# Kernel optimization log

Measured on AMD Instinct MI355X. Metric: run time of the kernel, lower is better.

The kernel has to match this reference:

```python
import jax, jax.numpy as jnp
import numpy as np

B, T, F, H = 2048, 50, 256, 256
PREVIOUS_VISIT = 50  # number of recurrence steps


def setup_inputs() -> dict:
    key = jax.random.key(0)
    k1, k2, k3, k4 = jax.random.split(key, 4)
    scale = 0.05  # keep gates in a sane range
    return {
        "input_context": jax.random.normal(k1, (B, T, F), dtype=jnp.float32),
        "W": jax.random.normal(k2, (F, 4 * H), dtype=jnp.float32) * scale,
        "U": jax.random.normal(k3, (H, 4 * H), dtype=jnp.float32) * scale,
        "b": jax.random.normal(k4, (4 * H,), dtype=jnp.float32) * scale,
    }


def reference(input_context, W, U, b):
    # Keras LSTMCell math, gate order i, f, g(cell candidate), o.
    batch = input_context.shape[0]
    hidden = U.shape[0]
    h0 = jnp.zeros((batch, hidden), dtype=input_context.dtype)
    c0 = jnp.zeros((batch, hidden), dtype=input_context.dtype)

    def step(carry, x_t):
        h, c = carry
        z = x_t @ W + h @ U + b  # [B, 4H]
        i, f, g, o = jnp.split(z, 4, axis=-1)
        i = jax.nn.sigmoid(i)
        f = jax.nn.sigmoid(f)
        g = jnp.tanh(g)
        o = jax.nn.sigmoid(o)
        c_new = f * c + i * g
        h_new = o * jnp.tanh(c_new)
        return (h_new, c_new), None

    # scan over time: [PV, B, F]
    xs = jnp.swapaxes(input_context[:, :PREVIOUS_VISIT, :], 0, 1)
    (h_fin, c_fin), _ = jax.lax.scan(step, (h0, c0), xs)
    # original returns (output_forward, state_forward=[h, c]); h == output
    return h_fin, c_fin
```

## Files before the change

### kernel.cpp

```cpp
#include <hip/hip_runtime.h>


#define B_ 2048
#define T_ 50
#define F_ 256
#define H_ 256
#define NZ 1024

typedef __attribute__((ext_vector_type(8))) short short8;
typedef __attribute__((ext_vector_type(4))) float f32x4;
typedef __attribute__((ext_vector_type(4))) int i32x4;
typedef unsigned short ushort_t;
typedef unsigned int uint_t;

__device__ __forceinline__ ushort_t f2bf(float f) {
    uint_t u = __float_as_uint(f);
    return (ushort_t)((u + 0x7FFFu + ((u >> 16) & 1u)) >> 16);
}
__device__ __forceinline__ uint_t pack2bf(float lo, float hi) {
    return (uint_t)f2bf(lo) | ((uint_t)f2bf(hi) << 16);
}
__device__ __forceinline__ float bf2f(ushort_t u) {
    return __uint_as_float(((uint_t)u) << 16);
}
__device__ __forceinline__ float sigm(float z) {
    return __builtin_amdgcn_rcpf(1.0f + __builtin_amdgcn_exp2f(z * -1.44269504f));
}
__device__ __forceinline__ float tanh_f(float z) {
    return 2.0f * __builtin_amdgcn_rcpf(1.0f + __builtin_amdgcn_exp2f(z * -2.88539008f)) - 1.0f;
}
__device__ __forceinline__ float xz_at(uint2 u, int j) {
    uint_t v = (j < 2) ? u.x : u.y;
    v = (j & 1) ? (v >> 16) : (v & 0xFFFFu);
    return bf2f((ushort_t)v);
}

__global__ void pack_w(const float* __restrict__ Wm, ushort_t* __restrict__ W2) {
    int gid  = blockIdx.x * 256 + threadIdx.x;
    int lane = gid & 63;
    int nf   = (gid >> 6) & 7;
    int w    = (gid >> 9) & 7;
    int kf   = (gid >> 12) & 7;
    int col = (nf >> 1) * 256 + w * 32 + (nf & 1) * 16 + (lane & 15);
    int kb  = kf * 32 + (lane >> 4) * 8;
    short8 v;
#pragma unroll
    for (int e = 0; e < 8; ++e)
        v[e] = (short)f2bf(Wm[(size_t)(kb + e) * NZ + col]);
    *(short8*)(W2 + ((((size_t)kf * 8 + w) * 8 + nf) * 64 + lane) * 8) = v;
}

__global__ void pack_scale(const float* __restrict__ Um,
                           float* __restrict__ scq, float* __restrict__ scd) {
    int j    = (blockIdx.x * 256 + threadIdx.x) >> 6;
    int lane = threadIdx.x & 63;
    float mx = 0.f;
#pragma unroll
    for (int i = 0; i < H_ / 64; ++i)
        mx = fmaxf(mx, fabsf(Um[(size_t)(i * 64 + lane) * NZ + j]));
#pragma unroll
    for (int off = 32; off; off >>= 1)
        mx = fmaxf(mx, __shfl_down(mx, off));
    if (lane == 0) {
        scq[j] = (mx > 0.f) ? (127.0f / mx) : 0.f;
        scd[j] = mx * (1.0f / 16129.0f);
    }
}

__global__ void pack_u8(const float* __restrict__ Um,
                        const float* __restrict__ scq, char* __restrict__ U8) {
    int gid  = blockIdx.x * 256 + threadIdx.x;
    int lane = gid & 63;
    int nf   = (gid >> 6) & 7;
    int w    = (gid >> 9) & 7;
    int kf   = (gid >> 12) & 3;
    int col = (nf >> 1) * 256 + w * 32 + (nf & 1) * 16 + (lane & 15);
    int k0  = kf * 64 + (lane >> 4) * 16;
    float qs = scq[col];
    union { char c[16]; int4 v; } u;
#pragma unroll
    for (int e = 0; e < 16; ++e)
        u.c[e] = (char)__float2int_rn(Um[(size_t)(k0 + e) * NZ + col] * qs);
    *(int4*)(U8 + (((size_t)(kf * 8 + w) * 8 + nf) << 10) + (size_t)lane * 16) = u.v;
}

__global__ __launch_bounds__(512, 2) void xw_gemm(
    const float* __restrict__ x, const float* __restrict__ bias,
    const ushort_t* __restrict__ W2, ushort_t* __restrict__ xz2) {
    __shared__ __align__(16) ushort_t As[64 * 256];

    const int tid = threadIdx.x;
    const int t = blockIdx.x, rb = blockIdx.y, row0 = rb * 64;
    const int w = tid >> 6, lane = tid & 63, r16 = lane & 15, q = lane >> 4;

    {
        int sr = tid >> 4, sc = tid & 15;
#pragma unroll
        for (int rr = 0; rr < 64; rr += 32) {
            const float* xp = x + ((size_t)(row0 + rr + sr) * T_ + t) * F_ + sc * 16;
            float4 f0 = *(const float4*)(xp + 0);
            float4 f1 = *(const float4*)(xp + 4);
            float4 f2 = *(const float4*)(xp + 8);
            float4 f3 = *(const float4*)(xp + 12);
            uint4 u0 = {pack2bf(f0.x, f0.y), pack2bf(f0.z, f0.w),
                        pack2bf(f1.x, f1.y), pack2bf(f1.z, f1.w)};
            uint4 u1 = {pack2bf(f2.x, f2.y), pack2bf(f2.z, f2.w),
                        pack2bf(f3.x, f3.y), pack2bf(f3.z, f3.w)};
            int c0 = (2 * sc) ^ (sr & 7), c1 = (2 * sc + 1) ^ (sr & 7);
            *(uint4*)&As[(rr + sr) * 256 + c0 * 8] = u0;
            *(uint4*)&As[(rr + sr) * 256 + c1 * 8] = u1;
        }
    }
    float bcol[8];
#pragma unroll
    for (int nf = 0; nf < 8; ++nf)
        bcol[nf] = bias[(nf >> 1) * 256 + w * 32 + (nf & 1) * 16 + r16];
    __syncthreads();

    f32x4 acc[4][8];
#pragma unroll
    for (int m = 0; m < 4; ++m)
#pragma unroll
        for (int nf = 0; nf < 8; ++nf) acc[m][nf] = (f32x4){0.f, 0.f, 0.f, 0.f};
    short8 SB0[8], SB1[8];

#define LOADB(BUF, KF_)                                                       \
    _Pragma("unroll") for (int nf = 0; nf < 8; ++nf)                          \
        BUF[nf] = *(const short8*)(W2 +                                       \
            ((((size_t)(KF_) * 8 + w) * 8 + nf) * 64 + lane) * 8);

#define MF1(BUF, KF_)                                                         \
    do {                                                                      \
        _Pragma("unroll") for (int m = 0; m < 4; ++m) {                       \
            short8 a_ = *(const short8*)&As[(m * 16 + r16) * 256              \
                                            + (((KF_)*4 + q) ^ (r16 & 7)) * 8];\
            _Pragma("unroll") for (int nf = 0; nf < 8; ++nf)                  \
                acc[m][nf] = __builtin_amdgcn_mfma_f32_16x16x32_bf16(         \
                    a_, BUF[nf], acc[m][nf], 0, 0, 0);                        \
        }                                                                     \
    } while (0)

    LOADB(SB0, 0); LOADB(SB1, 1);
    MF1(SB0, 0); LOADB(SB0, 2);
    MF1(SB1, 1); LOADB(SB1, 3);
    MF1(SB0, 2); LOADB(SB0, 4);
    MF1(SB1, 3); LOADB(SB1, 5);
    MF1(SB0, 4); LOADB(SB0, 6);
    MF1(SB1, 5); LOADB(SB1, 7);
    MF1(SB0, 6);
    MF1(SB1, 7);

    uint2* outp = (uint2*)xz2;
#pragma unroll
    for (int m = 0; m < 4; ++m) {
        const size_t cb = (((size_t)t * 64 + (size_t)(rb * 2 + (m >> 1))) * 8 + w) * 16
                        + (size_t)(m & 1) * 8;
#pragma unroll
        for (int nf = 0; nf < 8; ++nf) {
            f32x4 a = acc[m][nf];
            float b = bcol[nf];
            uint2 o = {pack2bf(a[0] + b, a[1] + b), pack2bf(a[2] + b, a[3] + b)};
            outp[(cb + nf) * 64 + lane] = o;
        }
    }
#undef LOADB
#undef MF1
}

__global__ __launch_bounds__(512, 1) void lstm_rec(
    const char* __restrict__ U8, const float* __restrict__ scd,
    const ushort_t* __restrict__ xz2, float* __restrict__ outp, int T) {
    __shared__ __align__(16) char UL[131072];
    __shared__ __align__(16) char hbc[2][4096];

    const int tid = threadIdx.x;
    const int rb = blockIdx.x, row0 = rb * 16;
    const int w = tid >> 6, lane = tid & 63, r16 = lane & 15, q = lane >> 4;

#pragma unroll
    for (int i = 0; i < 16; ++i) {
        int off = i * 8192 + tid * 16;
        __builtin_amdgcn_global_load_lds(
            (const __attribute__((address_space(1))) void*)(U8 + off),
            (__attribute__((address_space(3))) void*)(UL + off),
            16, 0, 0);
    }
    *(uint2*)&hbc[0][tid * 8] = (uint2){0, 0};

    i32x4 UA2[8], UA3[8];
#pragma unroll
    for (int nf = 0; nf < 8; ++nf)
        UA2[nf] = *(const i32x4*)(U8 + (((size_t)(2 * 8 + w) * 8 + nf) << 10)
                                  + (size_t)lane * 16);
#pragma unroll
    for (int nf = 0; nf < 8; ++nf)
        UA3[nf] = *(const i32x4*)(U8 + (((size_t)(3 * 8 + w) * 8 + nf) << 10)
                                  + (size_t)lane * 16);
#pragma unroll
    for (int nf = 0; nf < 8; ++nf) {
        asm volatile("" : "+a"(UA2[nf]));
        asm volatile("" : "+a"(UA3[nf]));
    }

    float d[8];
#pragma unroll
    for (int nf = 0; nf < 8; ++nf)
        d[nf] = scd[(nf >> 1) * 256 + w * 32 + (nf & 1) * 16 + r16];

    const uint2* xzp = (const uint2*)xz2;
    const size_t cbconst = (((size_t)(rb >> 1)) * 8 + w) * 16 + (size_t)(rb & 1) * 8;
    const uint2* xzb = xzp + cbconst * 64 + lane;
    const size_t TSTRIDE = (size_t)8192 * 64;

#define AFRAG8(HP_, KF_)                                                      \
    (*(const i32x4*)&(HP_)[r16 * 256 + ((((KF_)*4 + q) ^ (r16 & 7)) << 4)])

    i32x4 acc[8];
    f32x4 creg[2];
    creg[0] = (f32x4){0.f, 0.f, 0.f, 0.f};
    creg[1] = (f32x4){0.f, 0.f, 0.f, 0.f};
    f32x4 hreg[2];

    uint2 XZ[8];
#pragma unroll
    for (int k = 0; k < 8; ++k) XZ[k] = xzb[(size_t)k * 64];

    int cur = 0;
    __syncthreads();

#pragma clang loop unroll(disable)
    for (int t = 0; t < T; ++t) {
        const char* hc = hbc[cur];
        char* hn = hbc[cur ^ 1];

#pragma unroll
        for (int nf = 0; nf < 8; ++nf) {
            asm volatile("" : "+a"(UA2[nf]));
            asm volatile("" : "+a"(UA3[nf]));
        }

        uint2 XZn[8];
#pragma unroll
        for (int k = 0; k < 8; ++k)
            XZn[k] = xzb[(size_t)(t + 1) * TSTRIDE + (size_t)k * 64];

#pragma unroll
        for (int nf = 0; nf < 8; ++nf) acc[nf] = (i32x4){0, 0, 0, 0};

        __builtin_amdgcn_s_setprio(1);
#pragma unroll
        for (int kf = 0; kf < 2; ++kf) {
            i32x4 a = AFRAG8(hc, kf);
#pragma unroll
            for (int nf = 0; nf < 8; ++nf) {
                i32x4 b = *(const i32x4*)&UL[(((size_t)(kf * 8 + w) * 8 + nf) << 10)
                                             + (size_t)lane * 16];
                acc[nf] = __builtin_amdgcn_mfma_i32_16x16x64_i8(a, b, acc[nf], 0, 0, 0);
            }
        }
        {
            i32x4 a2 = AFRAG8(hc, 2);
#pragma unroll
            for (int nf = 0; nf < 8; ++nf)
                acc[nf] = __builtin_amdgcn_mfma_i32_16x16x64_i8(a2, UA2[nf], acc[nf], 0, 0, 0);
            i32x4 a3 = AFRAG8(hc, 3);
#pragma unroll
            for (int nf = 0; nf < 8; ++nf)
                acc[nf] = __builtin_amdgcn_mfma_i32_16x16x64_i8(a3, UA3[nf], acc[nf], 0, 0, 0);
        }
        __builtin_amdgcn_s_setprio(0);

#pragma unroll
        for (int hf = 0; hf < 2; ++hf) {
#pragma unroll
            for (int j = 0; j < 4; ++j) {
                float zi = (float)acc[0 + hf][j] * d[0 + hf] + xz_at(XZ[0 + hf], j);
                float zf = (float)acc[2 + hf][j] * d[2 + hf] + xz_at(XZ[2 + hf], j);
                float zg = (float)acc[4 + hf][j] * d[4 + hf] + xz_at(XZ[4 + hf], j);
                float zo = (float)acc[6 + hf][j] * d[6 + hf] + xz_at(XZ[6 + hf], j);
                float ig = sigm(zi);
                float fg = sigm(zf);
                float gg = tanh_f(zg);
                float og = sigm(zo);
                float cn = fg * creg[hf][j] + ig * gg;
                float hv = og * tanh_f(cn);
                creg[hf][j] = cn;
                hreg[hf][j] = hv;
                int row = q * 4 + j;
                int ch  = w * 32 + hf * 16 + r16;
                hn[row * 256 + (((ch >> 4) ^ (row & 7)) << 4) + (ch & 15)] =
                    (char)__float2int_rn(hv * 127.0f);
            }
        }

#pragma unroll
        for (int k = 0; k < 8; ++k) XZ[k] = XZn[k];

        asm volatile("s_waitcnt lgkmcnt(0)" ::: "memory");
        __builtin_amdgcn_s_barrier();
        cur ^= 1;
    }

#pragma unroll
    for (int hf = 0; hf < 2; ++hf) {
#pragma unroll
        for (int j = 0; j < 4; ++j) {
            int row = q * 4 + j;
            int ch  = w * 32 + hf * 16 + r16;
            size_t oi = (size_t)(row0 + row) * H_ + ch;
            outp[oi] = hreg[hf][j];
            outp[(size_t)B_ * H_ + oi] = creg[hf][j];
        }
    }
#undef AFRAG8
}

extern "C" void kernel_launch(void* const* d_in, const int* in_sizes, int n_in,
                              void* d_out, int out_size, void* d_ws, size_t ws_size,
                              hipStream_t stream) {
    const float* x    = (const float*)d_in[0];
    const float* Wm   = (const float*)d_in[1];
    const float* Um   = (const float*)d_in[2];
    const float* bias = (const float*)d_in[3];

    ushort_t* W2  = (ushort_t*)d_ws;
    char*     U8  = (char*)d_ws + 524288;
    float*    scq = (float*)((char*)d_ws + 786432);
    float*    scd = (float*)((char*)d_ws + 790528);
    ushort_t* xz2 = (ushort_t*)((char*)d_ws + 794624);

    pack_w<<<128, 256, 0, stream>>>(Wm, W2);
    pack_scale<<<256, 256, 0, stream>>>(Um, scq, scd);
    pack_u8<<<64, 256, 0, stream>>>(Um, scq, U8);
    dim3 g1(T_, 32);
    xw_gemm<<<g1, 512, 0, stream>>>(x, bias, W2, xz2);
    lstm_rec<<<128, 512, 0, stream>>>(U8, scd, xz2, (float*)d_out, T_);
}
```

Baseline: 224.1 us.

## Split recurrence into 8-row blocks over 256 workgroups with lane-shuffled gate epilogue

The recurrent kernel now gives each workgroup 8 batch rows instead of 16 and launches 256 workgroups instead of 128, so all compute units on the device are used. The MFMA still computes a 16-row tile, but rows 8-15 are duplicates of rows 0-7. A cross-half lane shuffle lets each lane handle one column with 4 rows, halving the per-lane gate math and XZ loads. The cost is half-wasted MFMA work per block, added shuffle latency on the serial critical path, and twice as many copies of U being loaded into LDS.

```diff
diff --git a/kernel.cpp b/kernel.cpp
--- a/kernel.cpp
+++ b/kernel.cpp
@@ -171,11 +171,15 @@
     const char* __restrict__ U8, const float* __restrict__ scd,
     const ushort_t* __restrict__ xz2, float* __restrict__ outp, int T) {
     __shared__ __align__(16) char UL[131072];
-    __shared__ __align__(16) char hbc[2][4096];
+    __shared__ __align__(16) char hbc[2][2048];
 
     const int tid = threadIdx.x;
-    const int rb = blockIdx.x, row0 = rb * 16;
-    const int w = tid >> 6, lane = tid & 63, r16 = lane & 15, q = lane >> 4;
+    const int rb = blockIdx.x;
+    const int w = tid >> 6, lane = tid & 63, r16 = lane & 15;
+    const int q  = lane >> 4;
+    const int hf = lane >> 5;
+    const int q2 = (lane >> 4) & 1;
+    const int r8 = r16 & 7;
 
 #pragma unroll
     for (int i = 0; i < 16; ++i) {
@@ -185,7 +189,7 @@
             (__attribute__((address_space(3))) void*)(UL + off),
             16, 0, 0);
     }
-    *(uint2*)&hbc[0][tid * 8] = (uint2){0, 0};
+    *(uint_t*)&hbc[0][tid * 4] = 0u;
 
     i32x4 UA2[8], UA3[8];
 #pragma unroll
@@ -202,28 +206,27 @@
         asm volatile("" : "+a"(UA3[nf]));
     }
 
-    float d[8];
-#pragma unroll
-    for (int nf = 0; nf < 8; ++nf)
-        d[nf] = scd[(nf >> 1) * 256 + w * 32 + (nf & 1) * 16 + r16];
+    const int mycol = w * 32 + hf * 16 + r16;
+    float d4[4];
+#pragma unroll
+    for (int g = 0; g < 4; ++g) d4[g] = scd[g * 256 + mycol];
 
     const uint2* xzp = (const uint2*)xz2;
-    const size_t cbconst = (((size_t)(rb >> 1)) * 8 + w) * 16 + (size_t)(rb & 1) * 8;
-    const uint2* xzb = xzp + cbconst * 64 + lane;
+    const size_t cb16 = (((size_t)(rb >> 2)) * 8 + w) * 16 + (size_t)((rb >> 1) & 1) * 8;
+    const int fq = ((rb & 1) << 1) + q2;
+    const uint2* xzb = xzp + (cb16 + hf) * 64 + fq * 16 + r16;
     const size_t TSTRIDE = (size_t)8192 * 64;
 
 #define AFRAG8(HP_, KF_)                                                      \
-    (*(const i32x4*)&(HP_)[r16 * 256 + ((((KF_)*4 + q) ^ (r16 & 7)) << 4)])
+    (*(const i32x4*)&(HP_)[r8 * 256 + ((((KF_)*4 + q) ^ r8) << 4)])
 
     i32x4 acc[8];
-    f32x4 creg[2];
-    creg[0] = (f32x4){0.f, 0.f, 0.f, 0.f};
-    creg[1] = (f32x4){0.f, 0.f, 0.f, 0.f};
-    f32x4 hreg[2];
-
-    uint2 XZ[8];
-#pragma unroll
-    for (int k = 0; k < 8; ++k) XZ[k] = xzb[(size_t)k * 64];
+    f32x4 creg = (f32x4){0.f, 0.f, 0.f, 0.f};
+    f32x4 hreg;
+
+    uint2 XZ[4];
+#pragma unroll
+    for (int g = 0; g < 4; ++g) XZ[g] = xzb[(size_t)g * 128];
 
     int cur = 0;
     __syncthreads();
@@ -239,10 +242,10 @@
             asm volatile("" : "+a"(UA3[nf]));
         }
 
-        uint2 XZn[8];
-#pragma unroll
-        for (int k = 0; k < 8; ++k)
-            XZn[k] = xzb[(size_t)(t + 1) * TSTRIDE + (size_t)k * 64];
+        uint2 XZn[4];
+#pragma unroll
+        for (int g = 0; g < 4; ++g)
+            XZn[g] = xzb[(size_t)(t + 1) * TSTRIDE + (size_t)g * 128];
 
 #pragma unroll
         for (int nf = 0; nf < 8; ++nf) acc[nf] = (i32x4){0, 0, 0, 0};
@@ -270,31 +273,37 @@
         }
         __builtin_amdgcn_s_setprio(0);
 
-#pragma unroll
-        for (int hf = 0; hf < 2; ++hf) {
+        i32x4 sa[4];
+#pragma unroll
+        for (int g = 0; g < 4; ++g) {
 #pragma unroll
             for (int j = 0; j < 4; ++j) {
-                float zi = (float)acc[0 + hf][j] * d[0 + hf] + xz_at(XZ[0 + hf], j);
-                float zf = (float)acc[2 + hf][j] * d[2 + hf] + xz_at(XZ[2 + hf], j);
-                float zg = (float)acc[4 + hf][j] * d[4 + hf] + xz_at(XZ[4 + hf], j);
-                float zo = (float)acc[6 + hf][j] * d[6 + hf] + xz_at(XZ[6 + hf], j);
-                float ig = sigm(zi);
-                float fg = sigm(zf);
-                float gg = tanh_f(zg);
-                float og = sigm(zo);
-                float cn = fg * creg[hf][j] + ig * gg;
-                float hv = og * tanh_f(cn);
-                creg[hf][j] = cn;
-                hreg[hf][j] = hv;
-                int row = q * 4 + j;
-                int ch  = w * 32 + hf * 16 + r16;
-                hn[row * 256 + (((ch >> 4) ^ (row & 7)) << 4) + (ch & 15)] =
-                    (char)__float2int_rn(hv * 127.0f);
+                int other = __shfl(acc[2 * g + 1][j], lane ^ 32, 64);
+                sa[g][j] = hf ? other : acc[2 * g][j];
             }
         }
 
 #pragma unroll
-        for (int k = 0; k < 8; ++k) XZ[k] = XZn[k];
+        for (int j = 0; j < 4; ++j) {
+            float zi = (float)sa[0][j] * d4[0] + xz_at(XZ[0], j);
+            float zf = (float)sa[1][j] * d4[1] + xz_at(XZ[1], j);
+            float zg = (float)sa[2][j] * d4[2] + xz_at(XZ[2], j);
+            float zo = (float)sa[3][j] * d4[3] + xz_at(XZ[3], j);
+            float ig = sigm(zi);
+            float fg = sigm(zf);
+            float gg = tanh_f(zg);
+            float og = sigm(zo);
+            float cn = fg * creg[j] + ig * gg;
+            float hv = og * tanh_f(cn);
+            creg[j] = cn;
+            hreg[j] = hv;
+            int row = q2 * 4 + j;
+            hn[row * 256 + (((mycol >> 4) ^ row) << 4) + (mycol & 15)] =
+                (char)__float2int_rn(hv * 127.0f);
+        }
+
+#pragma unroll
+        for (int g = 0; g < 4; ++g) XZ[g] = XZn[g];
 
         asm volatile("s_waitcnt lgkmcnt(0)" ::: "memory");
         __builtin_amdgcn_s_barrier();
@@ -302,15 +311,11 @@
     }
 
 #pragma unroll
-    for (int hf = 0; hf < 2; ++hf) {
-#pragma unroll
-        for (int j = 0; j < 4; ++j) {
-            int row = q * 4 + j;
-            int ch  = w * 32 + hf * 16 + r16;
-            size_t oi = (size_t)(row0 + row) * H_ + ch;
-            outp[oi] = hreg[hf][j];
-            outp[(size_t)B_ * H_ + oi] = creg[hf][j];
-        }
+    for (int j = 0; j < 4; ++j) {
+        int row = q2 * 4 + j;
+        size_t oi = (size_t)(rb * 8 + row) * H_ + mycol;
+        outp[oi] = hreg[j];
+        outp[(size_t)B_ * H_ + oi] = creg[j];
     }
 #undef AFRAG8
 }
@@ -334,5 +339,5 @@
     pack_u8<<<64, 256, 0, stream>>>(Um, scq, U8);
     dim3 g1(T_, 32);
     xw_gemm<<<g1, 512, 0, stream>>>(x, bias, W2, xz2);
-    lstm_rec<<<128, 512, 0, stream>>>(U8, scd, xz2, (float*)d_out, T_);
-}
+    lstm_rec<<<256, 512, 0, stream>>>(U8, scd, xz2, (float*)d_out, T_);
+}
```

Result: faster. 200.6 us (-10.5%).
